# Kernel optimization log

Measured on AMD Instinct MI355X. Metric: run time of the kernel, lower is better.

## Reference

```python
import jax, jax.numpy as jnp
import numpy as np

N, D, E, K = 16384, 512, 8, 2  # tokens, model dim, experts, top_k


def setup_inputs() -> dict:
    key = jax.random.key(0)
    k_x, k_l, k_w = jax.random.split(key, 3)
    input_batch = jax.random.normal(k_x, (N, D), dtype=jnp.float32)
    # Router-like top-k gates: distinct expert ids per token (matches the
    # module's assumption that each (token, slot) maps to a unique expert row).
    logits = jax.random.normal(k_l, (N, E), dtype=jnp.float32)
    top_vals, top_idx = jax.lax.top_k(logits, K)
    probabilities = jax.nn.softmax(top_vals, axis=-1)          # [N, K]
    indices = top_idx.astype(jnp.int32)                        # [N, K]
    W = jax.random.normal(k_w, (E, D, D), dtype=jnp.float32) * (1.0 / np.sqrt(D))
    b = jnp.zeros((E, D), dtype=jnp.float32)
    return {"input_batch": input_batch, "probabilities": probabilities,
            "indices": indices, "W": W, "b": b}


def reference(input_batch, probabilities, indices, W, b):
    # Original loops over experts, gathers tokens routed to each expert,
    # runs the expert, concatenates, restores original (token, slot) order,
    # applies AFTER_EXPERTS gate weighting, and sums over the top_k slots.
    # Equivalent vectorized math: out[n] = sum_k p[n,k] * expert_{idx[n,k]}(x[n]).
    y = jnp.einsum('nd,edo->eno', input_batch, W) + b[:, None, :]   # [E, N, D]
    n_ar = jnp.arange(input_batch.shape[0])[:, None]                # [N, 1]
    gathered = y[indices, n_ar]                                     # [N, K, D]
    output = jnp.sum(probabilities[..., None] * gathered, axis=1)   # [N, D]
    total_loss = jnp.float32(0.0)  # sampler_loss=0 (external indices), expert losses=0
    return output, total_loss
```

## Files before the change

kernel.cpp:

```cpp
#include <hip/hip_runtime.h>

#define NTOK 16384
#define DIM  512
#define NEXP 8
#define NPAIR 64
#define PCAP 8192

#define BM 128
#define BN 128
#define BK 32

typedef __bf16 bf16x8 __attribute__((ext_vector_type(8)));
typedef __bf16 bf16x4 __attribute__((ext_vector_type(4)));
typedef float  f32x4  __attribute__((ext_vector_type(4)));

__device__ __forceinline__ void async_cp16(const void* g, void* l) {
    __builtin_amdgcn_global_load_lds((const __attribute__((address_space(1))) void*)g,
                                     (__attribute__((address_space(3))) void*)l, 16, 0, 0);
}

__global__ __launch_bounds__(256) void k_prep(const float* __restrict__ W,
                                              __bf16* __restrict__ Wt,
                                              const float* __restrict__ x,
                                              __bf16* __restrict__ xb,
                                              const int* __restrict__ indices,
                                              const float* __restrict__ probs,
                                              int* __restrict__ cnt,
                                              int* __restrict__ tok_arr,
                                              float* __restrict__ plo_arr,
                                              float* __restrict__ phi_arr,
                                              float* __restrict__ out) {
    int b = blockIdx.x, tid = threadIdx.x;
    if (b < 2048) {
        __shared__ __bf16 tile[32][34];
        int e = b >> 8, rem = b & 255;
        int o0 = (rem >> 4) * 32, k0 = (rem & 15) * 32;
        const float* Wsrc = W + ((size_t)e * DIM + k0) * DIM + o0;
        for (int i = tid; i < 1024; i += 256) {
            int kk = i >> 5, oo = i & 31;
            tile[oo][kk] = (__bf16)Wsrc[(size_t)kk * DIM + oo];
        }
        __syncthreads();
        __bf16* dst = Wt + ((size_t)(e * 16 + (k0 >> 5)) * DIM + o0) * 32;
        for (int i = tid; i < 1024; i += 256) {
            int oo = i >> 5, kk = i & 31;
            dst[oo * 32 + kk] = tile[oo][kk];
        }
    } else if (b < 2304) {
        int base = (b - 2048) * 256 + tid;
        const float4* src = (const float4*)x;
        #pragma unroll
        for (int it = 0; it < 32; ++it) {
            int i = base + it * 65536;
            float4 v = src[i];
            bf16x4 h; h[0] = (__bf16)v.x; h[1] = (__bf16)v.y; h[2] = (__bf16)v.z; h[3] = (__bf16)v.w;
            *(bf16x4*)&xb[(size_t)i * 4] = h;
        }
    } else {
        __shared__ int lcnt[NPAIR], lbase[NPAIR];
        int t = (b - 2304) * 256 + tid;
        if (tid < NPAIR) lcnt[tid] = 0;
        __syncthreads();
        int   e0 = indices[2 * t], e1 = indices[2 * t + 1];
        float p0 = probs[2 * t],   p1 = probs[2 * t + 1];
        int lo = min(e0, e1), hi = max(e0, e1);
        float plo = (e0 < e1) ? p0 : p1;
        float phi = (e0 < e1) ? p1 : p0;
        int key = lo * 8 + hi;
        int lr = atomicAdd(&lcnt[key], 1);
        __syncthreads();
        if (tid < NPAIR) lbase[tid] = atomicAdd(&cnt[tid], lcnt[tid]);
        __syncthreads();
        int pos = lbase[key] + lr;
        if (pos < PCAP) {
            int q = key * PCAP + pos;
            tok_arr[q] = t; plo_arr[q] = plo; phi_arr[q] = phi;
        }
        if (b == 2304 && tid == 0) out[NTOK * DIM] = 0.0f;
    }
}

__global__ __launch_bounds__(256) void k_gemm(const __bf16* __restrict__ xb,
                                              const __bf16* __restrict__ Wt,
                                              const float* __restrict__ bias,
                                              const int* __restrict__ tok_arr,
                                              const float* __restrict__ plo_arr,
                                              const float* __restrict__ phi_arr,
                                              const int* __restrict__ cnt,
                                              float* __restrict__ out) {
    int p = blockIdx.x;
    int m_slot = (p >> 5) * 8 + (p & 7);
    int nt = (p >> 3) & 3;
    int key = -1, m_t = 0, count = 0, total = 0;
    for (int i = 0; i < NPAIR; ++i) {
        int c = cnt[i];
        int tl = (c + BM - 1) >> 7;
        if (key < 0 && m_slot < total + tl) { key = i; m_t = m_slot - total; count = c; }
        total += tl;
    }
    if (key < 0) return;
    if (count > PCAP) count = PCAP;
    int lo = key >> 3, hi = key & 7;
    int m0 = m_t * BM, n0 = nt * BN, tid = threadIdx.x;

    __shared__ __attribute__((aligned(16))) char smem[32768];
    __shared__ int   sTok[BM];
    __shared__ float sPlo[BM], sPhi[BM], sR[BM];

    if (tid < BM) {
        int g = m0 + tid;
        int tk = 0; float a = 0.f, h = 1e-30f;
        if (g < count) {
            int q = key * PCAP + g;
            tk = tok_arr[q]; a = plo_arr[q];
            float hv = phi_arr[q]; h = hv > 1e-30f ? hv : 1e-30f;
        }
        sTok[tid] = tk;
        sPlo[tid] = a; sPhi[tid] = h; sR[tid] = a / h;
    }
    __syncthreads();

    int wid  = tid >> 6, lane = tid & 63;
    int quad = lane >> 4, rr  = lane & 15;
    int wm = (wid >> 1) * 64, wn = (wid & 1) * 64;

    int rA0 = tid >> 2;
    int swz = ((tid & 3) ^ (rA0 & 3)) << 3;
    const __bf16* gA0 = xb + (size_t)sTok[rA0]      * DIM + swz;
    const __bf16* gA1 = xb + (size_t)sTok[rA0 + 64] * DIM + swz;
    size_t bOff = (size_t)((rA0 * 4 + ((tid & 3) ^ (rA0 & 3))) * 8);
    const __bf16* gBlo = Wt + ((size_t)(lo * 16) * DIM + n0) * 32 + bOff;
    const __bf16* gBhi = Wt + ((size_t)(hi * 16) * DIM + n0) * 32 + bOff;

    f32x4 acc[4][4] = {};

    async_cp16(gA0,         smem + tid * 16);
    async_cp16(gA1,         smem + tid * 16 + 4096);
    async_cp16(gBlo,        smem + 16384 + tid * 16);
    async_cp16(gBlo + 2048, smem + 16384 + tid * 16 + 4096);

    #pragma unroll 2
    for (int s = 0; s < 32; ++s) {
        int cur = s & 1;
        __syncthreads();
        if (s == 16) {
            #pragma unroll
            for (int i = 0; i < 4; ++i)
                #pragma unroll
                for (int reg = 0; reg < 4; ++reg) {
                    float rv = sR[wm + i * 16 + quad * 4 + reg];
                    #pragma unroll
                    for (int j = 0; j < 4; ++j) acc[i][j][reg] *= rv;
                }
        }
        if (s < 31) {
            int s1 = s + 1;
            int kt = s1 & 15, ka = kt * BK;
            const __bf16* gb = ((s1 < 16) ? gBlo : gBhi) + (size_t)kt * DIM * 32;
            char* dA = smem + (s1 & 1) * 8192;
            char* dB = smem + 16384 + (s1 & 1) * 8192;
            async_cp16(gA0 + ka,  dA + tid * 16);
            async_cp16(gA1 + ka,  dA + tid * 16 + 4096);
            async_cp16(gb,        dB + tid * 16);
            async_cp16(gb + 2048, dB + tid * 16 + 4096);
        }
        const __bf16* sA = (const __bf16*)(smem + cur * 8192);
        const __bf16* sB = (const __bf16*)(smem + 16384 + cur * 8192);
        bf16x8 af[4], bfr[4];
        int csw = (quad ^ (rr & 3)) * 8;
        #pragma unroll
        for (int i = 0; i < 4; ++i)
            af[i] = *(bf16x8*)&sA[(wm + i * 16 + rr) * BK + csw];
        #pragma unroll
        for (int j = 0; j < 4; ++j)
            bfr[j] = *(bf16x8*)&sB[(wn + j * 16 + rr) * BK + csw];
        #pragma unroll
        for (int i = 0; i < 4; ++i)
            #pragma unroll
            for (int j = 0; j < 4; ++j)
                acc[i][j] = __builtin_amdgcn_mfma_f32_16x16x32_bf16(af[i], bfr[j], acc[i][j], 0, 0, 0);
    }

    float blo[4], bhi[4];
    #pragma unroll
    for (int j = 0; j < 4; ++j) {
        blo[j] = bias[lo * DIM + n0 + wn + j * 16 + rr];
        bhi[j] = bias[hi * DIM + n0 + wn + j * 16 + rr];
    }
    #pragma unroll
    for (int i = 0; i < 4; ++i) {
        #pragma unroll
        for (int reg = 0; reg < 4; ++reg) {
            int row = wm + i * 16 + quad * 4 + reg;
            int g = m0 + row;
            if (g >= count) continue;
            int   tk = sTok[row];
            float ph = sPhi[row], pl = sPlo[row];
            float* dst = out + (size_t)tk * DIM + n0 + wn + rr;
            #pragma unroll
            for (int j = 0; j < 4; ++j)
                dst[j * 16] = acc[i][j][reg] * ph + pl * blo[j] + ph * bhi[j];
        }
    }
}

extern "C" void kernel_launch(void* const* d_in, const int* in_sizes, int n_in,
                              void* d_out, int out_size, void* d_ws, size_t ws_size,
                              hipStream_t stream) {
    const float* x    = (const float*)d_in[0];
    const float* prob = (const float*)d_in[1];
    const int*   idx  = (const int*)d_in[2];
    const float* W    = (const float*)d_in[3];
    const float* b    = (const float*)d_in[4];
    float* out = (float*)d_out;

    char* ws = (char*)d_ws;
    __bf16* Wt      = (__bf16*)ws;
    __bf16* xb      = (__bf16*)(ws + 4194304);
    int*    cnt     = (int*)   (ws + 4194304 + 16777216);
    int*    tok_arr = (int*)   (ws + 4194304 + 16777216 + 256);
    float*  plo_arr = (float*) (ws + 4194304 + 16777216 + 256 + 2097152);
    float*  phi_arr = (float*) (ws + 4194304 + 16777216 + 256 + 2 * 2097152);

    (void)hipMemsetAsync(cnt, 0, NPAIR * sizeof(int), stream);
    hipLaunchKernelGGL(k_prep, dim3(2368), dim3(256), 0, stream,
                       W, Wt, x, xb, idx, prob, cnt, tok_arr, plo_arr, phi_arr, out);
    hipLaunchKernelGGL(k_gemm, dim3(640), dim3(256), 0, stream,
                       xb, Wt, b, tok_arr, plo_arr, phi_arr, cnt, out);
}
```

Before: 143.9 us.

## Compute both expert GEMMs concurrently with separate accumulators, reusing A tile

Instead of running 32 k-steps over one accumulator and rescaling it by plo/phi halfway, the loop now runs 16 k-steps. Each step loads the A tile once and multiplies it against both experts' weight tiles into two accumulator sets, which are weighted separately in the epilogue. This halves A-tile global loads and LDS A reads, removes the mid-loop rescale and the division, and fixes precision issues when phi is tiny. The cost is double the accumulator registers (128 fp32 per thread) and 48KB of LDS, which may reduce occupancy or cause spills.

```diff
diff --git a/kernel.cpp b/kernel.cpp
--- a/kernel.cpp
+++ b/kernel.cpp
@@ -103,20 +103,19 @@
     int lo = key >> 3, hi = key & 7;
     int m0 = m_t * BM, n0 = nt * BN, tid = threadIdx.x;
 
-    __shared__ __attribute__((aligned(16))) char smem[32768];
+    __shared__ __attribute__((aligned(16))) char smem[49152];
     __shared__ int   sTok[BM];
-    __shared__ float sPlo[BM], sPhi[BM], sR[BM];
+    __shared__ float sPlo[BM], sPhi[BM];
 
     if (tid < BM) {
         int g = m0 + tid;
-        int tk = 0; float a = 0.f, h = 1e-30f;
+        int tk = 0; float a = 0.f, h = 0.f;
         if (g < count) {
             int q = key * PCAP + g;
-            tk = tok_arr[q]; a = plo_arr[q];
-            float hv = phi_arr[q]; h = hv > 1e-30f ? hv : 1e-30f;
+            tk = tok_arr[q]; a = plo_arr[q]; h = phi_arr[q];
         }
         sTok[tid] = tk;
-        sPlo[tid] = a; sPhi[tid] = h; sR[tid] = a / h;
+        sPlo[tid] = a; sPhi[tid] = h;
     }
     __syncthreads();
 
@@ -132,53 +131,53 @@
     const __bf16* gBlo = Wt + ((size_t)(lo * 16) * DIM + n0) * 32 + bOff;
     const __bf16* gBhi = Wt + ((size_t)(hi * 16) * DIM + n0) * 32 + bOff;
 
-    f32x4 acc[4][4] = {};
+    f32x4 accL[4][4] = {};
+    f32x4 accH[4][4] = {};
 
     async_cp16(gA0,         smem + tid * 16);
     async_cp16(gA1,         smem + tid * 16 + 4096);
     async_cp16(gBlo,        smem + 16384 + tid * 16);
     async_cp16(gBlo + 2048, smem + 16384 + tid * 16 + 4096);
+    async_cp16(gBhi,        smem + 32768 + tid * 16);
+    async_cp16(gBhi + 2048, smem + 32768 + tid * 16 + 4096);
 
     #pragma unroll 2
-    for (int s = 0; s < 32; ++s) {
-        int cur = s & 1;
-        __syncthreads();
-        if (s == 16) {
-            #pragma unroll
-            for (int i = 0; i < 4; ++i)
-                #pragma unroll
-                for (int reg = 0; reg < 4; ++reg) {
-                    float rv = sR[wm + i * 16 + quad * 4 + reg];
-                    #pragma unroll
-                    for (int j = 0; j < 4; ++j) acc[i][j][reg] *= rv;
-                }
-        }
-        if (s < 31) {
-            int s1 = s + 1;
-            int kt = s1 & 15, ka = kt * BK;
-            const __bf16* gb = ((s1 < 16) ? gBlo : gBhi) + (size_t)kt * DIM * 32;
-            char* dA = smem + (s1 & 1) * 8192;
-            char* dB = smem + 16384 + (s1 & 1) * 8192;
-            async_cp16(gA0 + ka,  dA + tid * 16);
-            async_cp16(gA1 + ka,  dA + tid * 16 + 4096);
-            async_cp16(gb,        dB + tid * 16);
-            async_cp16(gb + 2048, dB + tid * 16 + 4096);
-        }
-        const __bf16* sA = (const __bf16*)(smem + cur * 8192);
-        const __bf16* sB = (const __bf16*)(smem + 16384 + cur * 8192);
-        bf16x8 af[4], bfr[4];
+    for (int kt = 0; kt < 16; ++kt) {
+        int cur = kt & 1;
+        __syncthreads();
+        if (kt < 15) {
+            int ka = (kt + 1) * BK;
+            size_t wOff = (size_t)(kt + 1) * DIM * 32;
+            char* dA  = smem +         ((kt + 1) & 1) * 8192;
+            char* dBl = smem + 16384 + ((kt + 1) & 1) * 8192;
+            char* dBh = smem + 32768 + ((kt + 1) & 1) * 8192;
+            async_cp16(gA0 + ka,          dA  + tid * 16);
+            async_cp16(gA1 + ka,          dA  + tid * 16 + 4096);
+            async_cp16(gBlo + wOff,       dBl + tid * 16);
+            async_cp16(gBlo + wOff + 2048, dBl + tid * 16 + 4096);
+            async_cp16(gBhi + wOff,       dBh + tid * 16);
+            async_cp16(gBhi + wOff + 2048, dBh + tid * 16 + 4096);
+        }
+        const __bf16* sA  = (const __bf16*)(smem +         cur * 8192);
+        const __bf16* sBl = (const __bf16*)(smem + 16384 + cur * 8192);
+        const __bf16* sBh = (const __bf16*)(smem + 32768 + cur * 8192);
         int csw = (quad ^ (rr & 3)) * 8;
+        bf16x8 af[4], bl[4], bh[4];
         #pragma unroll
         for (int i = 0; i < 4; ++i)
             af[i] = *(bf16x8*)&sA[(wm + i * 16 + rr) * BK + csw];
         #pragma unroll
-        for (int j = 0; j < 4; ++j)
-            bfr[j] = *(bf16x8*)&sB[(wn + j * 16 + rr) * BK + csw];
+        for (int j = 0; j < 4; ++j) {
+            bl[j] = *(bf16x8*)&sBl[(wn + j * 16 + rr) * BK + csw];
+            bh[j] = *(bf16x8*)&sBh[(wn + j * 16 + rr) * BK + csw];
+        }
         #pragma unroll
         for (int i = 0; i < 4; ++i)
             #pragma unroll
-            for (int j = 0; j < 4; ++j)
-                acc[i][j] = __builtin_amdgcn_mfma_f32_16x16x32_bf16(af[i], bfr[j], acc[i][j], 0, 0, 0);
+            for (int j = 0; j < 4; ++j) {
+                accL[i][j] = __builtin_amdgcn_mfma_f32_16x16x32_bf16(af[i], bl[j], accL[i][j], 0, 0, 0);
+                accH[i][j] = __builtin_amdgcn_mfma_f32_16x16x32_bf16(af[i], bh[j], accH[i][j], 0, 0, 0);
+            }
     }
 
     float blo[4], bhi[4];
@@ -195,11 +194,11 @@
             int g = m0 + row;
             if (g >= count) continue;
             int   tk = sTok[row];
-            float ph = sPhi[row], pl = sPlo[row];
+            float pl = sPlo[row], ph = sPhi[row];
             float* dst = out + (size_t)tk * DIM + n0 + wn + rr;
             #pragma unroll
             for (int j = 0; j < 4; ++j)
-                dst[j * 16] = acc[i][j][reg] * ph + pl * blo[j] + ph * bhi[j];
+                dst[j * 16] = accL[i][j][reg] * pl + accH[i][j][reg] * ph + pl * blo[j] + ph * bhi[j];
         }
     }
 }
```

Measured after the change: 160.2 us. 1.11x slower.
